# Performance work log

Measured on AMD Instinct MI355X. Metric: run time of the kernel, lower is better.

The kernel has to match this reference:

```python
import jax, jax.numpy as jnp
import numpy as np

B, N, D, H, L, R = 2, 2048, 1024, 16, 3, 2
HID = int(D * 2.67)
NASH_ITERS, SINK_ITERS = 3, 10
EPS = 1e-6


def _rmsnorm(x, w):
    return x * w * jax.lax.rsqrt(jnp.mean(x * x, axis=-1, keepdims=True) + EPS)


def _sinkhorn(logits):
    # Sinkhorn-Knopp projection of exp(logits) to a doubly-stochastic matrix
    M = jnp.exp(logits)
    for _ in range(SINK_ITERS):
        M = M / jnp.sum(M, axis=1, keepdims=True)
        M = M / jnp.sum(M, axis=0, keepdims=True)
    return M


def _swiglu(x, wg, wu, wd):
    return (jax.nn.silu(x @ wg) * (x @ wu)) @ wd


def _attention(xl, wq, wk, Wv):
    # causal multi-head attention at one scale; V projection (Wv) is shared across scales
    b, n, d = xl.shape
    dh = d // H
    q = (xl @ wq).reshape(b, n, H, dh)
    k = (xl @ wk).reshape(b, n, H, dh)
    v = (xl @ Wv).reshape(b, n, H, dh)
    scores = jnp.einsum('bqhd,bkhd->bhqk', q, k) / jnp.asarray(float(np.sqrt(dh)), xl.dtype)
    mask = jnp.tril(jnp.ones((n, n), bool))
    scores = jnp.where(mask, scores, jnp.asarray(-1e9, xl.dtype))
    p = jax.nn.softmax(scores, axis=-1)
    return jnp.einsum('bhqk,bkhd->bqhd', p, v).reshape(b, n, d)


def _forward(x, norm_attn_w, norm_ffn_w, W_dec, Wq, Wk, Wv, Wo, agg_logits,
             w_gate, w_up, w_down, mhc_attn_logits, mhc_ffn_logits):
    residual = x
    xn = _rmsnorm(x, norm_attn_w)
    # 1) hierarchical decomposition: avg-pool by R each level, per-scale projection
    scales = []
    cur = xn
    for l in range(L):
        scales.append(cur @ W_dec[l])
        if l < L - 1:
            b, n, d = cur.shape
            cur = cur.reshape(b, n // R, R, d).mean(axis=2)
    # 2) multiscale causal attention with shared V; upsample back to N and project
    outs = []
    for l in range(L):
        o = _attention(scales[l], Wq[l], Wk[l], Wv)
        o = jnp.repeat(o, R ** l, axis=1)  # [B, N, D]
        outs.append(o @ Wo)
    Y = jnp.stack(outs, axis=0)  # [L, B, N, D]
    # 3) Nash aggregation: best-response iterations on scale weights
    w = jax.nn.softmax(agg_logits)
    for _ in range(NASH_ITERS):
        y_bar = jnp.einsum('l,lbnd->bnd', w, Y)
        u = -jnp.mean((Y - y_bar[None]) ** 2, axis=(1, 2, 3))  # [L] payoffs
        w = jax.nn.softmax(agg_logits + u)
    attn_out = jnp.einsum('l,lbnd->bnd', w, Y)
    aux_loss = jnp.sum(w * jnp.log(w * L + 1e-9))  # KL(w || uniform)
    # 4) mHC residual mixing (attention branch): doubly-stochastic convex mix
    P = _sinkhorn(mhc_attn_logits)
    x = P[0, 0] * residual + P[0, 1] * attn_out
    # 5) SwiGLU FFN + mHC residual (FFN branch)
    residual = x
    xn = _rmsnorm(x, norm_ffn_w)
    ffn_out = _swiglu(xn, w_gate, w_up, w_down)
    P2 = _sinkhorn(mhc_ffn_logits)
    x = P2[0, 0] * residual + P2[0, 1] * ffn_out
    return x, aux_loss


def setup_inputs() -> dict:
    key = jax.random.key(0)
    ks = jax.random.split(key, 16)
    init = 0.02
    s = lambda i, shape: jax.random.normal(ks[i], shape, jnp.float32) * init
    return {
        'x': jax.random.normal(ks[0], (B, N, D), jnp.float32),
        'norm_attn_w': jnp.ones((D,), jnp.float32),
        'norm_ffn_w': jnp.ones((D,), jnp.float32),
        'W_dec': s(1, (L, D, D)),
        'Wq': s(2, (L, D, D)),
        'Wk': s(3, (L, D, D)),
        'Wv': s(4, (D, D)),
        'Wo': s(5, (D, D)),
        'agg_logits': jnp.zeros((L,), jnp.float32),
        'w_gate': s(6, (D, HID)),
        'w_up': s(7, (D, HID)),
        'w_down': s(8, (HID, D)),
        'mhc_attn_logits': jnp.zeros((2, 2), jnp.float32),
        'mhc_ffn_logits': jnp.zeros((2, 2), jnp.float32),
    }


def reference(x, norm_attn_w, norm_ffn_w, W_dec, Wq, Wk, Wv, Wo, agg_logits,
              w_gate, w_up, w_down, mhc_attn_logits, mhc_ffn_logits):
    return _forward(x, norm_attn_w, norm_ffn_w, W_dec, Wq, Wk, Wv, Wo, agg_logits,
                    w_gate, w_up, w_down, mhc_attn_logits, mhc_ffn_logits)
```

## Files before the change

### kernel.cpp

```cpp
#include <hip/hip_runtime.h>
#include <stdint.h>


#define B_   2
#define N_   2048
#define D_   1024
#define H_   16
#define DH_  64
#define HID_ 2734
#define HIDP 2816
#define CNT  (B_*N_*D_)
#define LOG2E 1.4426950408889634f

typedef unsigned short u16;
typedef __attribute__((ext_vector_type(8))) short short8;
typedef __attribute__((ext_vector_type(4))) float f32x4;
typedef __attribute__((ext_vector_type(4))) uint16_t u16x4;

__device__ __forceinline__ u16 f2bf(float f) {
  uint32_t u = __builtin_bit_cast(uint32_t, f);
  u += 0x7fffu + ((u >> 16) & 1u);
  return (u16)(u >> 16);
}
__device__ __forceinline__ float bf2f(u16 h) {
  uint32_t u = ((uint32_t)h) << 16;
  return __builtin_bit_cast(float, u);
}
__device__ __forceinline__ uint32_t pkbf(float a, float b) {
  return (uint32_t)f2bf(a) | ((uint32_t)f2bf(b) << 16);
}
__device__ __forceinline__ void gload_lds16(const void* g, void* l) {
  __builtin_amdgcn_global_load_lds(
      (const __attribute__((address_space(1))) uint32_t*)g,
      (__attribute__((address_space(3))) uint32_t*)l, 16, 0, 0);
}

__global__ __launch_bounds__(256) void wprep_k(const float* __restrict__ Wdec, const float* __restrict__ Wq,
                                               const float* __restrict__ Wk, const float* __restrict__ Wv,
                                               const float* __restrict__ Wo, const float* __restrict__ Wg,
                                               const float* __restrict__ Wu, const float* __restrict__ Wdn,
                                               u16* __restrict__ A_wp, u16* __restrict__ WdecB,
                                               u16* __restrict__ WoT, u16* __restrict__ BTgu,
                                               u16* __restrict__ WdnT, float* __restrict__ SCb) {
  const int bid = blockIdx.x;
  if (bid >= 18688) {
    if (bid == 18688 && threadIdx.x < 64) SCb[threadIdx.x] = 0.f;
    int i = (bid - 18688)*1024 + threadIdx.x*4;
    float4 v = *(const float4*)(Wdec + i);
    u16x4 o; o[0]=f2bf(v.x); o[1]=f2bf(v.y); o[2]=f2bf(v.z); o[3]=f2bf(v.w);
    *(u16x4*)(WdecB + i) = o;
    return;
  }
  const float* src; u16* dst; int K, N, KP; float scale; int imode; int bx, by;
  if (bid < 9216) {
    int j = bid >> 10, t = bid & 1023; bx = t & 31; by = t >> 5;
    int l = j / 3, which = j - l*3;
    src = which==0 ? Wq + (size_t)l*1048576 : which==1 ? Wk + (size_t)l*1048576 : Wv;
    dst = A_wp + (size_t)(l*3072 + which*1024)*1024;
    K = 1024; N = 1024; KP = 1024; scale = (which==0) ? 0.125f*LOG2E : 1.f; imode = 0;
  } else if (bid < 10240) {
    int t = bid - 9216; bx = t & 31; by = t >> 5;
    src = Wo; dst = WoT; K=1024; N=1024; KP=1024; scale=1.f; imode=0;
  } else if (bid < 13056) {
    int t = bid - 10240; bx = t % 88; by = t / 88;
    src = Wg; dst = BTgu; K=1024; N=HID_; KP=1024; scale=1.f; imode=1;
  } else if (bid < 15872) {
    int t = bid - 13056; bx = t % 88; by = t / 88;
    src = Wu; dst = BTgu; K=1024; N=HID_; KP=1024; scale=1.f; imode=2;
  } else {
    int t = bid - 15872; bx = t & 31; by = t >> 5;
    src = Wdn; dst = WdnT; K=HID_; N=1024; KP=HIDP; scale=1.f; imode=0;
  }
  __shared__ float tt[32][33];
  const int tx = threadIdx.x & 31, ty = threadIdx.x >> 5;
  const int nb = bx*32, kb = by*32;
  #pragma unroll
  for (int i = 0; i < 4; i++) {
    int k = kb + ty + i*8, n = nb + tx;
    tt[ty + i*8][tx] = (k < K && n < N) ? src[(size_t)k * N + n] * scale : 0.f;
  }
  __syncthreads();
  #pragma unroll
  for (int i = 0; i < 4; i++) {
    int n = nb + ty + i*8, k = kb + tx;
    int r;
    if (imode == 0) r = n;
    else if (imode == 1) r = ((n>>4)<<5) + (n&15);
    else r = ((n>>4)<<5) + 16 + (n&15);
    dst[(size_t)r * KP + k] = f2bf(tt[tx][ty + i*8]);
  }
}

__global__ __launch_bounds__(256) void rmsA_k(const float* __restrict__ x, const float* __restrict__ w,
                                              u16* __restrict__ xn, u16* __restrict__ xp1) {
  const int j = blockIdx.x;
  const float* xr0 = x + (size_t)(2*j) * D_;
  const float* xr1 = xr0 + D_;
  float a0[4], a1[4], wv[4];
  float ss0 = 0.f, ss1 = 0.f;
  #pragma unroll
  for (int i = 0; i < 4; i++) {
    int c = threadIdx.x + i*256;
    a0[i] = xr0[c]; a1[i] = xr1[c]; wv[i] = w[c];
    ss0 += a0[i]*a0[i]; ss1 += a1[i]*a1[i];
  }
  #pragma unroll
  for (int o = 1; o < 64; o <<= 1) { ss0 += __shfl_xor(ss0, o); ss1 += __shfl_xor(ss1, o); }
  __shared__ float r0[4], r1[4];
  if ((threadIdx.x & 63) == 0) { r0[threadIdx.x >> 6] = ss0; r1[threadIdx.x >> 6] = ss1; }
  __syncthreads();
  float sc0 = rsqrtf((r0[0]+r0[1]+r0[2]+r0[3]) * (1.f/D_) + 1e-6f);
  float sc1 = rsqrtf((r1[0]+r1[1]+r1[2]+r1[3]) * (1.f/D_) + 1e-6f);
  #pragma unroll
  for (int i = 0; i < 4; i++) {
    int c = threadIdx.x + i*256;
    float xa = a0[i]*wv[i]*sc0, xb = a1[i]*wv[i]*sc1;
    xn[(size_t)(2*j)*D_ + c]     = f2bf(xa);
    xn[(size_t)(2*j)*D_ + D_ + c] = f2bf(xb);
    xp1[(size_t)j*D_ + c] = f2bf(0.5f*(xa + xb));
  }
}

__global__ __launch_bounds__(256) void pool_k(const u16* __restrict__ in, u16* __restrict__ out, int lg) {
  const int No = 1 << lg;
  const int total4 = B_ * No * 256;
  for (int i = blockIdx.x*256 + threadIdx.x; i < total4; i += gridDim.x*256) {
    int d4 = i & 255; int j = (i >> 8) & (No - 1); int b = i >> (8 + lg);
    size_t src = ((size_t)(b*2*No + 2*j) << 10) + d4*4;
    u16x4 a = *(const u16x4*)(in + src);
    u16x4 c = *(const u16x4*)(in + src + 1024);
    u16x4 o;
    #pragma unroll
    for (int t = 0; t < 4; t++) o[t] = f2bf(0.5f * (bf2f(a[t]) + bf2f(c[t])));
    *(u16x4*)(out + (size_t)i*4) = o;
  }
}

template<int MT, int MODE>
__global__ __launch_bounds__(256) void gemm_t(const u16* __restrict__ A, const u16* __restrict__ BT,
                                              void* __restrict__ Cv, const float* __restrict__ X1,
                                              const float* __restrict__ SCp,
                                              int N, int K, int t1, int t2, unsigned int bt_stride) {
  __shared__ __align__(16) u16 As[MT*32*32];
  __shared__ __align__(16) u16 Bs[128*32];
  const int tid = threadIdx.x;
  const int lane = tid & 63, wid = tid >> 6;
  const int quad = lane >> 4, c16 = lane & 15;
  const int y = blockIdx.y;
  const int m0 = y * (MT*32), n0 = blockIdx.x * 128;
  const int wm = wid >> 1, wn = wid & 1;
  const int level = (y >= t2) ? 2 : ((y >= t1) ? 1 : 0);
  BT += (size_t)level * bt_stride;

  f32x4 acc[MT][4];
  #pragma unroll
  for (int i = 0; i < MT; i++)
    #pragma unroll
    for (int j = 0; j < 4; j++) acc[i][j] = f32x4{0.f,0.f,0.f,0.f};

  const int srow = lane >> 2;
  const int schunk = lane & 3;
  for (int k0 = 0; k0 < K; k0 += 32) {
    #pragma unroll
    for (int t = 0; t < MT/2; t++) {
      int idx = wid*(MT/2) + t;
      int row = idx*16 + srow;
      int g = (schunk ^ ((row >> 1) & 3)) * 8;
      gload_lds16(A + (size_t)(m0+row)*K + k0 + g, As + idx*512);
    }
    #pragma unroll
    for (int t = 0; t < 2; t++) {
      int idx = wid*2 + t;
      int row = idx*16 + srow;
      int g = (schunk ^ ((row >> 1) & 3)) * 8;
      gload_lds16(BT + (size_t)(n0+row)*K + k0 + g, Bs + idx*512);
    }
    __syncthreads();
    short8 af[MT], bfr[4];
    #pragma unroll
    for (int mt = 0; mt < MT; mt++) {
      int ar = wm*(MT*16) + mt*16 + c16;
      af[mt]  = *(const short8*)(As + ar*32 + (quad ^ ((ar>>1)&3))*8);
    }
    #pragma unroll
    for (int nt = 0; nt < 4; nt++) {
      int br = wn*64 + nt*16 + c16;
      bfr[nt] = *(const short8*)(Bs + br*32 + (quad ^ ((br>>1)&3))*8);
    }
    #pragma unroll
    for (int mt = 0; mt < MT; mt++)
      #pragma unroll
      for (int nt = 0; nt < 4; nt++)
        acc[mt][nt] = __builtin_amdgcn_mfma_f32_16x16x32_bf16(af[mt], bfr[nt], acc[mt][nt], 0, 0, 0);
    __syncthreads();
  }
  if (MODE == 1) {
    u16* C = (u16*)Cv;
    #pragma unroll
    for (int mt = 0; mt < MT; mt++)
      #pragma unroll
      for (int nt = 0; nt < 4; nt++)
        #pragma unroll
        for (int r = 0; r < 4; r++) {
          int row = m0 + wm*(MT*16) + mt*16 + quad*4 + r;
          int col = n0 + wn*64 + nt*16 + c16;
          C[(size_t)row * N + col] = f2bf(acc[mt][nt][r]);
        }
  } else if (MODE == 2) {
    float* C = (float*)Cv;
    const float q0 = SCp[11], q1 = SCp[12];
    #pragma unroll
    for (int mt = 0; mt < MT; mt++)
      #pragma unroll
      for (int nt = 0; nt < 4; nt++)
        #pragma unroll
        for (int r = 0; r < 4; r++) {
          int row = m0 + wm*(MT*16) + mt*16 + quad*4 + r;
          int col = n0 + wn*64 + nt*16 + c16;
          size_t o = (size_t)row * N + col;
          C[o] = q0 * X1[o] + q1 * acc[mt][nt][r];
        }
  } else {
    u16* Hc = (u16*)Cv;
    const int hbase = (n0 >> 1) + wn*32;
    #pragma unroll
    for (int mt = 0; mt < MT; mt++)
      #pragma unroll
      for (int r = 0; r < 4; r++) {
        int row = m0 + wm*(MT*16) + mt*16 + quad*4 + r;
        #pragma unroll
        for (int pr = 0; pr < 2; pr++) {
          float g = acc[mt][2*pr][r], u = acc[mt][2*pr+1][r];
          float h = g / (1.f + __expf(-g)) * u;
          Hc[(size_t)row * HIDP + hbase + pr*16 + c16] = f2bf(h);
        }
      }
  }
}

__global__ __launch_bounds__(256) void vtrans_k(const u16* __restrict__ QKV, u16* __restrict__ VTa) {
  __shared__ u16 t[32][33];
  const int bid = blockIdx.x;
  int level, tt2;
  if (bid < 4096)      { level = 0; tt2 = bid; }
  else if (bid < 6144) { level = 1; tt2 = bid - 4096; }
  else                 { level = 2; tt2 = bid - 6144; }
  const int Nl = 2048 >> level;
  const int ntiles = Nl >> 5;
  const int b = tt2 / (ntiles*32);
  const int rem = tt2 - b*(ntiles*32);
  const int c0 = (rem / ntiles) * 32;
  const int n0 = (rem - (rem / ntiles)*ntiles) * 32;
  const int rowbase = (level==0) ? 0 : (level==1) ? 4096 : 6144;
  const size_t vtoff = (level==0) ? 0 : (level==1) ? 4194304 : 6291456;
  const u16* in = QKV + (size_t)rowbase*3072 + 2048;
  u16* out = VTa + vtoff;
  const int tx = threadIdx.x & 31, ty = threadIdx.x >> 5;
  #pragma unroll
  for (int i = 0; i < 4; i++)
    t[ty + i*8][tx] = in[(size_t)(b*Nl + n0 + ty + i*8)*3072 + c0 + tx];
  __syncthreads();
  #pragma unroll
  for (int i = 0; i < 4; i++)
    out[(size_t)(b*1024 + c0 + ty + i*8)*Nl + n0 + tx] = t[tx][ty + i*8];
}

__global__ __launch_bounds__(256) void flash_k(const u16* __restrict__ QKVg,
                                               const u16* __restrict__ VTg,
                                               u16* __restrict__ Og) {
  __shared__ __align__(16) u16 Kt[2][64*64];
  __shared__ __align__(16) u16 Vt[2][64*64];
  __shared__ __align__(16) u16 Ps[4][32*68];
  const int tid = threadIdx.x, lane = tid & 63, wid = tid >> 6;
  const int quad = lane >> 4, c16 = lane & 15;
  const int id = blockIdx.x;
  int qt, bh, Nl, rowbase; size_t vtoff;
  if (id < 512)      { qt = 15 - (id >> 5);            bh = id & 31;  Nl = 2048; rowbase = 0;    vtoff = 0; }
  else if (id < 768) { int t2 = id - 512; qt = 7 - (t2 >> 5); bh = t2 & 31; Nl = 1024; rowbase = 4096; vtoff = 4194304; }
  else               { int t2 = id - 768; qt = 3 - (t2 >> 5); bh = t2 & 31; Nl = 512;  rowbase = 6144; vtoff = 6291456; }
  const int b = bh >> 4, h = bh & 15;
  const u16* QK = QKVg + ((size_t)(rowbase + b*Nl)) * 3072 + h*64;
  u16* Ow = Og + ((size_t)(rowbase + b*Nl)) * 1024 + h*64;
  const u16* VT = VTg + vtoff + ((size_t)b*1024 + h*64) * (size_t)Nl;

  const int q0r = qt*128 + wid*32;
  short8 bq[2][2];
  #pragma unroll
  for (int qh = 0; qh < 2; qh++) {
    const u16* qp = QK + (size_t)(q0r + qh*16 + c16)*3072 + quad*8;
    bq[qh][0] = *(const short8*)qp;
    bq[qh][1] = *(const short8*)(qp + 32);
  }
  const int si0 = wid*2, si1 = si0 + 1;
  const int sr0 = si0*8 + (lane>>3), sr1 = si1*8 + (lane>>3);
  const int sg  = ((lane&7) ^ (lane>>3)) * 8;
  const u16* Ks0 = QK + 1024 + (size_t)sr0*3072 + sg;
  const u16* Ks1 = QK + 1024 + (size_t)sr1*3072 + sg;
  const u16* Vs0 = VT + (size_t)sr0*Nl + sg;
  const u16* Vs1 = VT + (size_t)sr1*Nl + sg;

  f32x4 oacc[2][4];
  f32x4 lacc[2];
  #pragma unroll
  for (int qh = 0; qh < 2; qh++) {
    lacc[qh] = f32x4{0.f,0.f,0.f,0.f};
    #pragma unroll
    for (int nt = 0; nt < 4; nt++) oacc[qh][nt] = f32x4{0.f,0.f,0.f,0.f};
  }

  auto stage = [&](int kt, int p) {
    const size_t ko = (size_t)kt * 64;
    gload_lds16(Ks0 + ko*3072, &Kt[p][si0*512]);
    gload_lds16(Ks1 + ko*3072, &Kt[p][si1*512]);
    gload_lds16(Vs0 + ko,      &Vt[p][si0*512]);
    gload_lds16(Vs1 + ko,      &Vt[p][si1*512]);
  };
  const int kmax_w = 2*qt + (wid >> 1);
  const int ktot   = 2*qt + 2;
  stage(0, 0);

  for (int kt = 0; kt < ktot; kt++) {
    const int p = kt & 1;
    __syncthreads();
    if (kt + 1 < ktot) stage(kt+1, p^1);
    if (kt > kmax_w) continue;

    f32x4 st[2][4];
    #pragma unroll
    for (int nt = 0; nt < 4; nt++) {
      int key = nt*16 + c16, x = key & 7;
      short8 a0 = *(const short8*)(&Kt[p][key*64 + ((quad    ) ^ x)*8]);
      short8 a1 = *(const short8*)(&Kt[p][key*64 + ((quad + 4) ^ x)*8]);
      #pragma unroll
      for (int qh = 0; qh < 2; qh++) {
        f32x4 s = f32x4{0.f,0.f,0.f,0.f};
        s = __builtin_amdgcn_mfma_f32_16x16x32_bf16(a0, bq[qh][0], s, 0, 0, 0);
        s = __builtin_amdgcn_mfma_f32_16x16x32_bf16(a1, bq[qh][1], s, 0, 0, 0);
        st[qh][nt] = s;
      }
    }
    if (kt >= 2*qt) {
      const int kb = kt*64;
      #pragma unroll
      for (int qh = 0; qh < 2; qh++) {
        const int qr = q0r + qh*16 + c16;
        #pragma unroll
        for (int nt = 0; nt < 4; nt++) {
          #pragma unroll
          for (int r = 0; r < 4; r++) {
            float e = __builtin_amdgcn_exp2f(st[qh][nt][r]);
            st[qh][nt][r] = (kb + nt*16 + quad*4 + r <= qr) ? e : 0.f;
          }
          lacc[qh] += st[qh][nt];
        }
      }
    } else {
      #pragma unroll
      for (int qh = 0; qh < 2; qh++)
        #pragma unroll
        for (int nt = 0; nt < 4; nt++) {
          #pragma unroll
          for (int r = 0; r < 4; r++) st[qh][nt][r] = __builtin_amdgcn_exp2f(st[qh][nt][r]);
          lacc[qh] += st[qh][nt];
        }
    }
    #pragma unroll
    for (int qh = 0; qh < 2; qh++) {
      const int prow = qh*16 + c16;
      #pragma unroll
      for (int nt = 0; nt < 4; nt++) {
        uint2 pk;
        pk.x = pkbf(st[qh][nt][0], st[qh][nt][1]);
        pk.y = pkbf(st[qh][nt][2], st[qh][nt][3]);
        *(uint2*)(&Ps[wid][prow*68 + nt*16 + quad*4]) = pk;
      }
    }
    short8 bp[2][2];
    #pragma unroll
    for (int qh = 0; qh < 2; qh++) {
      bp[qh][0] = *(const short8*)(&Ps[wid][(qh*16 + c16)*68 +      quad*8]);
      bp[qh][1] = *(const short8*)(&Ps[wid][(qh*16 + c16)*68 + 32 + quad*8]);
    }
    #pragma unroll
    for (int nt = 0; nt < 4; nt++) {
      int dh = nt*16 + c16, x = dh & 7;
      short8 a0 = *(const short8*)(&Vt[p][dh*64 + ((quad    ) ^ x)*8]);
      short8 a1 = *(const short8*)(&Vt[p][dh*64 + ((quad + 4) ^ x)*8]);
      #pragma unroll
      for (int qh = 0; qh < 2; qh++) {
        oacc[qh][nt] = __builtin_amdgcn_mfma_f32_16x16x32_bf16(a0, bp[qh][0], oacc[qh][nt], 0, 0, 0);
        oacc[qh][nt] = __builtin_amdgcn_mfma_f32_16x16x32_bf16(a1, bp[qh][1], oacc[qh][nt], 0, 0, 0);
      }
    }
  }
  #pragma unroll
  for (int qh = 0; qh < 2; qh++) {
    float ls = lacc[qh][0] + lacc[qh][1] + lacc[qh][2] + lacc[qh][3];
    ls += __shfl_xor(ls, 16);
    ls += __shfl_xor(ls, 32);
    const float rl = 1.f / ls;
    #pragma unroll
    for (int nt = 0; nt < 4; nt++) {
      uint2 o;
      o.x = pkbf(oacc[qh][nt][0]*rl, oacc[qh][nt][1]*rl);
      o.y = pkbf(oacc[qh][nt][2]*rl, oacc[qh][nt][3]*rl);
      *(uint2*)(Ow + (size_t)(q0r + qh*16 + c16)*1024 + nt*16 + quad*4) = o;
    }
  }
}

__global__ __launch_bounds__(256) void gram_k(const u16* __restrict__ Y0, const u16* __restrict__ Y1,
                                              const u16* __restrict__ Y2, float* __restrict__ G) {
  float a[6] = {0,0,0,0,0,0};
  const int total4 = CNT/4;
  for (int i = blockIdx.x*256 + threadIdx.x; i < total4; i += gridDim.x*256) {
    int d4 = i & 255; int n = (i >> 8) & (N_-1); int b = i >> 19;
    u16x4 y0v = *(const u16x4*)(Y0 + (size_t)i*4);
    u16x4 y1v = *(const u16x4*)(Y1 + (((size_t)(b*1024 + (n>>1))) << 10) + d4*4);
    u16x4 y2v = *(const u16x4*)(Y2 + (((size_t)(b*512  + (n>>2))) << 10) + d4*4);
    #pragma unroll
    for (int t = 0; t < 4; t++) {
      float y0 = bf2f(y0v[t]), y1 = bf2f(y1v[t]), y2 = bf2f(y2v[t]);
      a[0] += y0*y0; a[1] += y0*y1; a[2] += y0*y2;
      a[3] += y1*y1; a[4] += y1*y2; a[5] += y2*y2;
    }
  }
  __shared__ float red[4][6];
  const int lane = threadIdx.x & 63, wid = threadIdx.x >> 6;
  #pragma unroll
  for (int t = 0; t < 6; t++) {
    float v = a[t];
    v += __shfl_xor(v, 1);  v += __shfl_xor(v, 2);  v += __shfl_xor(v, 4);
    v += __shfl_xor(v, 8);  v += __shfl_xor(v, 16); v += __shfl_xor(v, 32);
    a[t] = v;
  }
  if (lane == 0)
    #pragma unroll
    for (int t = 0; t < 6; t++) red[wid][t] = a[t];
  __syncthreads();
  if (threadIdx.x < 6)
    atomicAdd(&G[threadIdx.x], red[0][threadIdx.x] + red[1][threadIdx.x] +
                               red[2][threadIdx.x] + red[3][threadIdx.x]);
}

__global__ void head_k(float* SC, const float* __restrict__ agg, const float* __restrict__ mA,
                       const float* __restrict__ mF, float* __restrict__ aux_out) {
  if (threadIdx.x != 0 || blockIdx.x != 0) return;
  float G[6];
  for (int t = 0; t < 6; t++) G[t] = SC[t];
  const int gi[3][3] = {{0,1,2},{1,3,4},{2,4,5}};
  float a[3] = {agg[0], agg[1], agg[2]};
  float w[3];
  {
    float m = fmaxf(a[0], fmaxf(a[1], a[2])); float s = 0.f;
    for (int l = 0; l < 3; l++) { w[l] = expf(a[l]-m); s += w[l]; }
    for (int l = 0; l < 3; l++) w[l] /= s;
  }
  const float inv = 1.f / (float)CNT;
  for (int it = 0; it < 3; it++) {
    float q = 0.f;
    for (int l = 0; l < 3; l++) for (int m2 = 0; m2 < 3; m2++) q += w[l]*w[m2]*G[gi[l][m2]];
    float z[3];
    for (int l = 0; l < 3; l++) {
      float dot = w[0]*G[gi[l][0]] + w[1]*G[gi[l][1]] + w[2]*G[gi[l][2]];
      z[l] = a[l] - (G[gi[l][l]] - 2.f*dot + q) * inv;
    }
    float m = fmaxf(z[0], fmaxf(z[1], z[2])); float s = 0.f;
    for (int l = 0; l < 3; l++) { w[l] = expf(z[l]-m); s += w[l]; }
    for (int l = 0; l < 3; l++) w[l] /= s;
  }
  SC[6] = w[0]; SC[7] = w[1]; SC[8] = w[2];
  aux_out[0] = w[0]*logf(w[0]*3.f + 1e-9f) + w[1]*logf(w[1]*3.f + 1e-9f) + w[2]*logf(w[2]*3.f + 1e-9f);
  for (int which = 0; which < 2; which++) {
    const float* Lg = which ? mF : mA;
    float M0 = expf(Lg[0]), M1 = expf(Lg[1]), M2 = expf(Lg[2]), M3 = expf(Lg[3]);
    for (int i2 = 0; i2 < 10; i2++) {
      float r0 = M0+M1, r1 = M2+M3; M0 /= r0; M1 /= r0; M2 /= r1; M3 /= r1;
      float c0 = M0+M2, c1 = M1+M3; M0 /= c0; M2 /= c0; M1 /= c1; M3 /= c1;
    }
    SC[9 + which*2] = M0; SC[10 + which*2] = M1;
  }
}

__global__ __launch_bounds__(256) void mixrms_k(const float* __restrict__ x, const u16* __restrict__ Y0,
                                                const u16* __restrict__ Y1, const u16* __restrict__ Y2,
                                                const float* __restrict__ SC, const float* __restrict__ w2,
                                                float* __restrict__ x1, u16* __restrict__ xn2) {
  const float w0 = SC[6], w1 = SC[7], ww2 = SC[8], p0 = SC[9], p1 = SC[10];
  const int i = blockIdx.x;
  const int b = i >> 11, n = i & 2047;
  const float* xr = x + (size_t)i * D_;
  const u16* y0 = Y0 + (size_t)i * D_;
  const u16* y1 = Y1 + (size_t)(b*1024 + (n>>1)) * D_;
  const u16* y2 = Y2 + (size_t)(b*512  + (n>>2)) * D_;
  float xv[4], wv[4];
  float ss = 0.f;
  #pragma unroll
  for (int t = 0; t < 4; t++) {
    int c = threadIdx.x + t*256;
    float v = p0*xr[c] + p1*(w0*bf2f(y0[c]) + w1*bf2f(y1[c]) + ww2*bf2f(y2[c]));
    xv[t] = v; wv[t] = w2[c]; ss += v*v;
    x1[(size_t)i*D_ + c] = v;
  }
  #pragma unroll
  for (int o = 1; o < 64; o <<= 1) ss += __shfl_xor(ss, o);
  __shared__ float red[4];
  if ((threadIdx.x & 63) == 0) red[threadIdx.x >> 6] = ss;
  __syncthreads();
  float sc = rsqrtf((red[0]+red[1]+red[2]+red[3]) * (1.f/D_) + 1e-6f);
  #pragma unroll
  for (int t = 0; t < 4; t++) {
    int c = threadIdx.x + t*256;
    xn2[(size_t)i*D_ + c] = f2bf(xv[t]*wv[t]*sc);
  }
}

extern "C" void kernel_launch(void* const* d_in, const int* in_sizes, int n_in,
                              void* d_out, int out_size, void* d_ws, size_t ws_size,
                              hipStream_t stream) {
  (void)in_sizes; (void)n_in; (void)out_size; (void)ws_size;
  const float* x    = (const float*)d_in[0];
  const float* nw1  = (const float*)d_in[1];
  const float* nw2  = (const float*)d_in[2];
  const float* Wdec = (const float*)d_in[3];
  const float* Wq   = (const float*)d_in[4];
  const float* Wk   = (const float*)d_in[5];
  const float* Wv   = (const float*)d_in[6];
  const float* Wo   = (const float*)d_in[7];
  const float* agg  = (const float*)d_in[8];
  const float* Wg   = (const float*)d_in[9];
  const float* Wu   = (const float*)d_in[10];
  const float* Wdn  = (const float*)d_in[11];
  const float* mA   = (const float*)d_in[12];
  const float* mF   = (const float*)d_in[13];
  float* out = (float*)d_out;

  char* ws = (char*)d_ws;
  size_t off = 0;
  auto take = [&](size_t b) { size_t r = off; off += (b + 255) & ~(size_t)255; return r; };

  u16* A_wp  = (u16*)(ws + take((size_t)9216*1024*2));
  u16* WdecB = (u16*)(ws + take((size_t)3*1024*1024*2));
  u16* Wqkv  = (u16*)(ws + take((size_t)9216*1024*2));
  u16* BTgu  = (u16*)(ws + take((size_t)5632*1024*2));
  u16* WdnT  = (u16*)(ws + take((size_t)HIDP*1024*2));
  u16* WoT   = (u16*)(ws + take((size_t)1024*1024*2));
  u16* xn_all = (u16*)(ws + take((size_t)7168*1024*2));
  float* x1  = (float*)(ws + take((size_t)CNT*4));
  float* SCb = (float*)(ws + take(256));
  char*  big = ws + take(88080384);
  u16*   QKV   = (u16*)big;
  u16*   VTa   = (u16*)(big + 44040192);
  u16*   Ob    = (u16*)(big + 58720256);
  u16*   YC    = (u16*)(big + 73400320);
  u16*   hbuf  = (u16*)big;

  dim3 blk(256);
  const int BIG = 1 << 30;

  wprep_k<<<21760, blk, 0, stream>>>(Wdec, Wq, Wk, Wv, Wo, Wg, Wu, Wdn,
                                     A_wp, WdecB, WoT, BTgu, WdnT, SCb);
  gemm_t<4,1><<<dim3(8, 72), blk, 0, stream>>>(A_wp, WdecB, Wqkv, nullptr, nullptr,
                                               1024, 1024, 24, 48, 1024u*1024u);
  rmsA_k<<<2048, blk, 0, stream>>>(x, nw1, xn_all, xn_all + (size_t)4096*1024);
  pool_k<<<512, blk, 0, stream>>>(xn_all + (size_t)4096*1024, xn_all + (size_t)6144*1024, 9);
  gemm_t<4,1><<<dim3(24, 56), blk, 0, stream>>>(xn_all, Wqkv, QKV, nullptr, nullptr,
                                                3072, 1024, 32, 48, 3072u*1024u);
  vtrans_k<<<7168, blk, 0, stream>>>(QKV, VTa);
  flash_k<<<896, blk, 0, stream>>>(QKV, VTa, Ob);
  gemm_t<2,1><<<dim3(8, 112), blk, 0, stream>>>(Ob, WoT, YC, nullptr, nullptr,
                                                1024, 1024, BIG, BIG, 0u);
  u16* YC1 = YC + (size_t)4096*1024;
  u16* YC2 = YC + (size_t)6144*1024;
  gram_k<<<1024, blk, 0, stream>>>(YC, YC1, YC2, SCb);
  head_k<<<1, 64, 0, stream>>>(SCb, agg, mA, mF, out + CNT);
  mixrms_k<<<4096, blk, 0, stream>>>(x, YC, YC1, YC2, SCb, nw2, x1, xn_all);
  gemm_t<4,3><<<dim3(44, 32), blk, 0, stream>>>(xn_all, BTgu, hbuf, nullptr, nullptr,
                                                5632, 1024, BIG, BIG, 0u);
  gemm_t<2,2><<<dim3(8, 64), blk, 0, stream>>>(hbuf, WdnT, out, x1, SCb,
                                               1024, HIDP, BIG, BIG, 0u);
}
```

Before: 503.2 us.

## Deepen GEMM K-tile to 64, enlarge M tiles, fuse V transpose into QKV epilogue

The GEMM kernel now stages 64-wide K slices with an 8-way XOR swizzle, which halves the number of barrier-separated iterations. M tiles are enlarged (MT up to 8) and the launch grids are shrunk to match, with launch_bounds raised to two blocks per CU. A new epilogue mode writes the V columns of the QKV projection directly in transposed layout, so the separate vtrans kernel is removed. wprep also zeroes a few padding rows of the gate/up weights. Larger tiles improve data reuse but raise register and LDS pressure and leave fewer blocks to fill the GPU. The transposed epilogue's 8-byte strided stores may be poorly coalesced.

```diff
diff --git a/kernel.cpp b/kernel.cpp
--- a/kernel.cpp
+++ b/kernel.cpp
@@ -43,6 +43,13 @@
                                                u16* __restrict__ WoT, u16* __restrict__ BTgu,
                                                u16* __restrict__ WdnT, float* __restrict__ SCb) {
   const int bid = blockIdx.x;
+  if (bid >= 21760) {
+    int bid0 = bid - 21760;
+    int row = (bid0 < 2) ? (5454 + bid0) : (5470 + (bid0 - 2));
+    u16x4 zz; zz[0]=0; zz[1]=0; zz[2]=0; zz[3]=0;
+    *(u16x4*)(BTgu + (size_t)row*1024 + threadIdx.x*4) = zz;
+    return;
+  }
   if (bid >= 18688) {
     if (bid == 18688 && threadIdx.x < 64) SCb[threadIdx.x] = 0.f;
     int i = (bid - 18688)*1024 + threadIdx.x*4;
@@ -137,12 +144,13 @@
 }
 
 template<int MT, int MODE>
-__global__ __launch_bounds__(256) void gemm_t(const u16* __restrict__ A, const u16* __restrict__ BT,
-                                              void* __restrict__ Cv, const float* __restrict__ X1,
-                                              const float* __restrict__ SCp,
-                                              int N, int K, int t1, int t2, unsigned int bt_stride) {
-  __shared__ __align__(16) u16 As[MT*32*32];
-  __shared__ __align__(16) u16 Bs[128*32];
+__global__ __launch_bounds__(256, 2) void gemm_t(const u16* __restrict__ A, const u16* __restrict__ BT,
+                                                 void* __restrict__ Cv, void* __restrict__ Cv2,
+                                                 const float* __restrict__ X1,
+                                                 const float* __restrict__ SCp,
+                                                 int N, int K, int t1, int t2, unsigned int bt_stride) {
+  __shared__ __align__(16) u16 As[MT*32*64];
+  __shared__ __align__(16) u16 Bs[128*64];
   const int tid = threadIdx.x;
   const int lane = tid & 63, wid = tid >> 6;
   const int quad = lane >> 4, c16 = lane & 15;
@@ -158,40 +166,45 @@
     #pragma unroll
     for (int j = 0; j < 4; j++) acc[i][j] = f32x4{0.f,0.f,0.f,0.f};
 
-  const int srow = lane >> 2;
-  const int schunk = lane & 3;
-  for (int k0 = 0; k0 < K; k0 += 32) {
-    #pragma unroll
-    for (int t = 0; t < MT/2; t++) {
-      int idx = wid*(MT/2) + t;
-      int row = idx*16 + srow;
-      int g = (schunk ^ ((row >> 1) & 3)) * 8;
+  const int srow = lane >> 3;
+  const int schunk = lane & 7;
+  for (int k0 = 0; k0 < K; k0 += 64) {
+    #pragma unroll
+    for (int t = 0; t < MT; t++) {
+      int idx = wid*MT + t;
+      int row = idx*8 + srow;
+      int g = (schunk ^ (row & 7)) * 8;
       gload_lds16(A + (size_t)(m0+row)*K + k0 + g, As + idx*512);
     }
     #pragma unroll
-    for (int t = 0; t < 2; t++) {
-      int idx = wid*2 + t;
-      int row = idx*16 + srow;
-      int g = (schunk ^ ((row >> 1) & 3)) * 8;
+    for (int t = 0; t < 4; t++) {
+      int idx = wid*4 + t;
+      int row = idx*8 + srow;
+      int g = (schunk ^ (row & 7)) * 8;
       gload_lds16(BT + (size_t)(n0+row)*K + k0 + g, Bs + idx*512);
     }
     __syncthreads();
-    short8 af[MT], bfr[4];
-    #pragma unroll
-    for (int mt = 0; mt < MT; mt++) {
-      int ar = wm*(MT*16) + mt*16 + c16;
-      af[mt]  = *(const short8*)(As + ar*32 + (quad ^ ((ar>>1)&3))*8);
-    }
-    #pragma unroll
-    for (int nt = 0; nt < 4; nt++) {
-      int br = wn*64 + nt*16 + c16;
-      bfr[nt] = *(const short8*)(Bs + br*32 + (quad ^ ((br>>1)&3))*8);
-    }
-    #pragma unroll
-    for (int mt = 0; mt < MT; mt++)
-      #pragma unroll
-      for (int nt = 0; nt < 4; nt++)
-        acc[mt][nt] = __builtin_amdgcn_mfma_f32_16x16x32_bf16(af[mt], bfr[nt], acc[mt][nt], 0, 0, 0);
+    #pragma unroll
+    for (int kh = 0; kh < 2; kh++) {
+      short8 af[MT], bfr[4];
+      #pragma unroll
+      for (int mt = 0; mt < MT; mt++) {
+        int ar = wm*(MT*16) + mt*16 + c16;
+        int ck = (kh*4 + quad) ^ (ar & 7);
+        af[mt] = *(const short8*)(As + ar*64 + ck*8);
+      }
+      #pragma unroll
+      for (int nt = 0; nt < 4; nt++) {
+        int br = wn*64 + nt*16 + c16;
+        int ck = (kh*4 + quad) ^ (br & 7);
+        bfr[nt] = *(const short8*)(Bs + br*64 + ck*8);
+      }
+      #pragma unroll
+      for (int mt = 0; mt < MT; mt++)
+        #pragma unroll
+        for (int nt = 0; nt < 4; nt++)
+          acc[mt][nt] = __builtin_amdgcn_mfma_f32_16x16x32_bf16(af[mt], bfr[nt], acc[mt][nt], 0, 0, 0);
+    }
     __syncthreads();
   }
   if (MODE == 1) {
@@ -220,7 +233,7 @@
           size_t o = (size_t)row * N + col;
           C[o] = q0 * X1[o] + q1 * acc[mt][nt][r];
         }
-  } else {
+  } else if (MODE == 3) {
     u16* Hc = (u16*)Cv;
     const int hbase = (n0 >> 1) + wn*32;
     #pragma unroll
@@ -235,34 +248,41 @@
           Hc[(size_t)row * HIDP + hbase + pr*16 + c16] = f2bf(h);
         }
       }
-  }
-}
-
-__global__ __launch_bounds__(256) void vtrans_k(const u16* __restrict__ QKV, u16* __restrict__ VTa) {
-  __shared__ u16 t[32][33];
-  const int bid = blockIdx.x;
-  int level, tt2;
-  if (bid < 4096)      { level = 0; tt2 = bid; }
-  else if (bid < 6144) { level = 1; tt2 = bid - 4096; }
-  else                 { level = 2; tt2 = bid - 6144; }
-  const int Nl = 2048 >> level;
-  const int ntiles = Nl >> 5;
-  const int b = tt2 / (ntiles*32);
-  const int rem = tt2 - b*(ntiles*32);
-  const int c0 = (rem / ntiles) * 32;
-  const int n0 = (rem - (rem / ntiles)*ntiles) * 32;
-  const int rowbase = (level==0) ? 0 : (level==1) ? 4096 : 6144;
-  const size_t vtoff = (level==0) ? 0 : (level==1) ? 4194304 : 6291456;
-  const u16* in = QKV + (size_t)rowbase*3072 + 2048;
-  u16* out = VTa + vtoff;
-  const int tx = threadIdx.x & 31, ty = threadIdx.x >> 5;
-  #pragma unroll
-  for (int i = 0; i < 4; i++)
-    t[ty + i*8][tx] = in[(size_t)(b*Nl + n0 + ty + i*8)*3072 + c0 + tx];
-  __syncthreads();
-  #pragma unroll
-  for (int i = 0; i < 4; i++)
-    out[(size_t)(b*1024 + c0 + ty + i*8)*Nl + n0 + tx] = t[tx][ty + i*8];
+  } else {
+    if (n0 < 2048) {
+      u16* C = (u16*)Cv;
+      #pragma unroll
+      for (int mt = 0; mt < MT; mt++)
+        #pragma unroll
+        for (int nt = 0; nt < 4; nt++)
+          #pragma unroll
+          for (int r = 0; r < 4; r++) {
+            int row = m0 + wm*(MT*16) + mt*16 + quad*4 + r;
+            int col = n0 + wn*64 + nt*16 + c16;
+            C[(size_t)row * N + col] = f2bf(acc[mt][nt][r]);
+          }
+    } else {
+      const int Nl = 2048 >> level;
+      const int lvbase = (level==0) ? 0 : (level==1) ? 4096 : 6144;
+      const size_t vtoff = (level==0) ? 0 : (level==1) ? 4194304 : 6291456;
+      u16* VT = (u16*)Cv2 + vtoff;
+      #pragma unroll
+      for (int mt = 0; mt < MT; mt++) {
+        int rowg = m0 + wm*(MT*16) + mt*16 + quad*4;
+        int nloc = rowg - lvbase;
+        int b = nloc / Nl;
+        int n = nloc - b*Nl;
+        #pragma unroll
+        for (int nt = 0; nt < 4; nt++) {
+          int c = n0 - 2048 + wn*64 + nt*16 + c16;
+          u16x4 o;
+          o[0]=f2bf(acc[mt][nt][0]); o[1]=f2bf(acc[mt][nt][1]);
+          o[2]=f2bf(acc[mt][nt][2]); o[3]=f2bf(acc[mt][nt][3]);
+          *(u16x4*)(VT + ((size_t)(b*1024 + c))*Nl + n) = o;
+        }
+      }
+    }
+  }
 }
 
 __global__ __launch_bounds__(256) void flash_k(const u16* __restrict__ QKVg,
@@ -558,25 +578,24 @@
   dim3 blk(256);
   const int BIG = 1 << 30;
 
-  wprep_k<<<21760, blk, 0, stream>>>(Wdec, Wq, Wk, Wv, Wo, Wg, Wu, Wdn,
+  wprep_k<<<21924, blk, 0, stream>>>(Wdec, Wq, Wk, Wv, Wo, Wg, Wu, Wdn,
                                      A_wp, WdecB, WoT, BTgu, WdnT, SCb);
-  gemm_t<4,1><<<dim3(8, 72), blk, 0, stream>>>(A_wp, WdecB, Wqkv, nullptr, nullptr,
-                                               1024, 1024, 24, 48, 1024u*1024u);
+  gemm_t<8,1><<<dim3(8, 36), blk, 0, stream>>>(A_wp, WdecB, Wqkv, nullptr, nullptr, nullptr,
+                                               1024, 1024, 12, 24, 1024u*1024u);
   rmsA_k<<<2048, blk, 0, stream>>>(x, nw1, xn_all, xn_all + (size_t)4096*1024);
   pool_k<<<512, blk, 0, stream>>>(xn_all + (size_t)4096*1024, xn_all + (size_t)6144*1024, 9);
-  gemm_t<4,1><<<dim3(24, 56), blk, 0, stream>>>(xn_all, Wqkv, QKV, nullptr, nullptr,
-                                                3072, 1024, 32, 48, 3072u*1024u);
-  vtrans_k<<<7168, blk, 0, stream>>>(QKV, VTa);
+  gemm_t<8,4><<<dim3(24, 28), blk, 0, stream>>>(xn_all, Wqkv, QKV, VTa, nullptr, nullptr,
+                                                3072, 1024, 16, 24, 3072u*1024u);
   flash_k<<<896, blk, 0, stream>>>(QKV, VTa, Ob);
-  gemm_t<2,1><<<dim3(8, 112), blk, 0, stream>>>(Ob, WoT, YC, nullptr, nullptr,
-                                                1024, 1024, BIG, BIG, 0u);
+  gemm_t<8,1><<<dim3(8, 28), blk, 0, stream>>>(Ob, WoT, YC, nullptr, nullptr, nullptr,
+                                               1024, 1024, BIG, BIG, 0u);
   u16* YC1 = YC + (size_t)4096*1024;
   u16* YC2 = YC + (size_t)6144*1024;
   gram_k<<<1024, blk, 0, stream>>>(YC, YC1, YC2, SCb);
   head_k<<<1, 64, 0, stream>>>(SCb, agg, mA, mF, out + CNT);
   mixrms_k<<<4096, blk, 0, stream>>>(x, YC, YC1, YC2, SCb, nw2, x1, xn_all);
-  gemm_t<4,3><<<dim3(44, 32), blk, 0, stream>>>(xn_all, BTgu, hbuf, nullptr, nullptr,
+  gemm_t<8,3><<<dim3(44, 16), blk, 0, stream>>>(xn_all, BTgu, hbuf, nullptr, nullptr, nullptr,
                                                 5632, 1024, BIG, BIG, 0u);
-  gemm_t<2,2><<<dim3(8, 64), blk, 0, stream>>>(hbuf, WdnT, out, x1, SCb,
+  gemm_t<4,2><<<dim3(8, 32), blk, 0, stream>>>(hbuf, WdnT, out, nullptr, x1, SCb,
                                                1024, HIDP, BIG, BIG, 0u);
 }
```

Measured after the change: 499.1 us. Within noise of the previous version (-0.8%).
